# Optimization experiments

Hardware: AMD Instinct MI355X
Metric: run time of the kernel (lower is better)

## Reference

```python
import jax, jax.numpy as jnp
import numpy as np

N, E, D, L, G = 50000, 1600000, 128, 3, 64


def setup_inputs() -> dict:
    key = jax.random.key(0)
    ks = jax.random.split(key, 10)
    s = 1.0 / np.sqrt(D).astype(np.float32)
    X = jax.random.normal(ks[0], (N, D), jnp.float32)
    edge_index = jax.random.randint(ks[1], (2, E), 0, N, dtype=jnp.int32)
    edge_types = jax.random.randint(ks[2], (E,), 0, 2, dtype=jnp.int32)
    batch_ids = jnp.sort(jax.random.randint(ks[3], (N,), 0, G, dtype=jnp.int32))
    Wd = jax.random.uniform(ks[4], (L, D, D), jnp.float32, -s, s)
    bd = jax.random.uniform(ks[5], (L, D), jnp.float32, -s, s)
    Wc = jax.random.uniform(ks[6], (L, D, D), jnp.float32, -s, s)
    bc = jax.random.uniform(ks[7], (L, D), jnp.float32, -s, s)
    Ws = jax.random.uniform(ks[8], (L, D, D), jnp.float32, -s, s)
    bs = jax.random.uniform(ks[9], (L, D), jnp.float32, -s, s)
    return dict(X=X, Wd=Wd, bd=bd, Wc=Wc, bc=bc, Ws=Ws, bs=bs,
                edge_index=edge_index, edge_types=edge_types, batch_ids=batch_ids)


def reference(X, Wd, bd, Wc, bc, Ws, bs, edge_index, edge_types, batch_ids):
    src, dst = edge_index[0], edge_index[1]
    is_data = (edge_types == 0)[:, None]  # [E,1] edge-type selector
    for l in range(L):
        # Linear commutes with gather: compute node-level GEMMs once,
        # then per-edge gather + type select (same math as per-edge Linear).
        Xd = X @ Wd[l] + bd[l]            # [N,D] data-edge messages
        Xc = X @ Wc[l] + bc[l]            # [N,D] control-edge messages
        msg = jnp.where(is_data, Xd[src], Xc[src])      # [E,D]
        agg = jax.ops.segment_sum(msg, dst, num_segments=N)  # scatter-add
        X = jax.nn.relu(agg + X @ Ws[l] + bs[l])
    # global mean pool per graph
    sums = jax.ops.segment_sum(X, batch_ids, num_segments=G)
    cnts = jax.ops.segment_sum(jnp.ones((N,), X.dtype), batch_ids, num_segments=G)
    return sums / jnp.maximum(cnts, 1.0)[:, None]
```

## Files before the change

kernel.cpp:

```cpp
#include <hip/hip_runtime.h>
#include <hip/hip_fp16.h>

#define N_NODES 50000
#define N_EDGES 1600000
#define DIM     128
#define NLAYERS 3
#define NGRAPHS 64

#define NBUCK   196
#define CSR_BLKS 256
#define EPB     (N_EDGES / CSR_BLKS)
#define EITER   ((EPB + 255) / 256)

typedef _Float16 half8 __attribute__((ext_vector_type(8)));
typedef float    f32x4 __attribute__((ext_vector_type(4)));
typedef float    f32x2 __attribute__((ext_vector_type(2)));

#define LDK 136

__global__ __launch_bounds__(256) void setup_kernel(
        const float* __restrict__ X, __half* __restrict__ Xh,
        const float* __restrict__ Wd, const float* __restrict__ Wc,
        const float* __restrict__ Ws, __half* __restrict__ WT,
        float* __restrict__ sums, int* __restrict__ gcnt) {
    int i = blockIdx.x * 256 + threadIdx.x;
    if (i < N_NODES * DIM / 4) {
        float4 v = *(const float4*)(X + (size_t)i * 4);
        union { __half2 h2[2]; uint2 u; } pk;
        pk.h2[0] = __floats2half2_rn(v.x, v.y);
        pk.h2[1] = __floats2half2_rn(v.z, v.w);
        *(uint2*)(Xh + (size_t)i * 4) = pk.u;
    }
    if (i < 9 * DIM * DIM) {
        int k  = i & 127;
        int n  = (i >> 7) & 127;
        int lw = i >> 14;
        int l  = lw / 3, w = lw - 3 * l;
        const float* W = ((w == 0) ? Wd : (w == 1) ? Wc : Ws)
                         + (size_t)l * DIM * DIM;
        WT[i] = __float2half(W[k * DIM + n]);
    }
    if (i < NGRAPHS * DIM) sums[i] = 0.f;
    if (i < NGRAPHS) gcnt[i] = 0;
}

__global__ __launch_bounds__(256) void csr1_kernel(const int* __restrict__ dst,
                                                   int* __restrict__ cntmat) {
    __shared__ int hc[NBUCK];
    int tid = threadIdx.x;
    for (int i = tid; i < NBUCK; i += 256) hc[i] = 0;
    __syncthreads();
    int base = blockIdx.x * EPB;
#pragma unroll
    for (int i = 0; i < EITER; ++i) {
        int idx = i * 256 + tid;
        if (idx < EPB) atomicAdd(&hc[dst[base + idx] >> 8], 1);
    }
    __syncthreads();
    for (int i = tid; i < NBUCK; i += 256)
        cntmat[i * CSR_BLKS + blockIdx.x] = hc[i];
}

__global__ __launch_bounds__(256) void scanA_kernel(const int* __restrict__ cntmat,
                                                    int* __restrict__ exc,
                                                    int* __restrict__ btot) {
    __shared__ int sh[256];
    int tid = threadIdx.x, b = blockIdx.x;
    int v = cntmat[b * CSR_BLKS + tid];
    sh[tid] = v;
    __syncthreads();
    for (int o = 1; o < 256; o <<= 1) {
        int t = (tid >= o) ? sh[tid - o] : 0;
        __syncthreads();
        sh[tid] += t;
        __syncthreads();
    }
    exc[b * CSR_BLKS + tid] = sh[tid] - v;
    if (tid == 255) btot[b] = sh[255];
}

__global__ __launch_bounds__(256) void csr2_kernel(const int* __restrict__ src,
                                                   const int* __restrict__ dst,
                                                   const int* __restrict__ et,
                                                   const int* __restrict__ exc,
                                                   const int* __restrict__ btot,
                                                   int* __restrict__ bstart,
                                                   int* __restrict__ esv) {
    __shared__ int sh[256];
    __shared__ int bst[NBUCK];
    __shared__ int cur[NBUCK];
    int tid = threadIdx.x;
    int v = (tid < NBUCK) ? btot[tid] : 0;
    sh[tid] = v;
    __syncthreads();
    for (int o = 1; o < 256; o <<= 1) {
        int t = (tid >= o) ? sh[tid - o] : 0;
        __syncthreads();
        sh[tid] += t;
        __syncthreads();
    }
    if (tid < NBUCK) bst[tid] = sh[tid] - v;
    if (blockIdx.x == 0) {
        if (tid < NBUCK) bstart[tid] = sh[tid] - v;
        if (tid == NBUCK - 1) bstart[NBUCK] = sh[tid];
    }
    __syncthreads();
    if (tid < NBUCK) cur[tid] = exc[tid * CSR_BLKS + blockIdx.x] + bst[tid];
    __syncthreads();
    int base = blockIdx.x * EPB;
#pragma unroll
    for (int i = 0; i < EITER; ++i) {
        int idx = i * 256 + tid;
        if (idx < EPB) {
            int e = base + idx;
            int d = dst[e];
            int pos = atomicAdd(&cur[d >> 8], 1);
            esv[pos] = (src[e] + et[e] * N_NODES) | ((d & 255) << 17);
        }
    }
}

__global__ __launch_bounds__(256) void csr3_kernel(const int* __restrict__ esv,
                                                   const int* __restrict__ bstart,
                                                   int* __restrict__ col,
                                                   int* __restrict__ row_start,
                                                   int* __restrict__ deg) {
    __shared__ int cnt[256];
    __shared__ int sh[256];
    __shared__ int cur[256];
    int tid = threadIdx.x, b = blockIdx.x;
    int bs = bstart[b], be = bstart[b + 1];
    cnt[tid] = 0;
    __syncthreads();
    for (int e = bs + tid; e < be; e += 256)
        atomicAdd(&cnt[(esv[e] >> 17) & 255], 1);
    __syncthreads();
    int v = cnt[tid];
    sh[tid] = v;
    __syncthreads();
    for (int o = 1; o < 256; o <<= 1) {
        int t = (tid >= o) ? sh[tid - o] : 0;
        __syncthreads();
        sh[tid] += t;
        __syncthreads();
    }
    int off  = sh[tid] - v;
    int node = (b << 8) + tid;
    if (node < N_NODES) {
        row_start[node] = bs + off;
        deg[node]       = v;
    }
    cur[tid] = bs + off;
    __syncthreads();
    for (int e = bs + tid; e < be; e += 256) {
        int pk  = esv[e];
        int nd  = (pk >> 17) & 255;
        int pos = atomicAdd(&cur[nd], 1);
        col[pos] = pk & 0x1FFFF;
    }
}

__global__ __launch_bounds__(256) void gemm3m_kernel(
        const __half* __restrict__ Xh,
        const __half* __restrict__ WTl,
        const float* __restrict__ bd, const float* __restrict__ bc,
        const float* __restrict__ bs,
        unsigned char* __restrict__ Od, unsigned char* __restrict__ Oc,
        __half* __restrict__ Sh) {
    __shared__ _Float16 As[64 * LDK];
    __shared__ _Float16 Bs[128 * LDK];

    const int tid = threadIdx.x;
    const int m0  = blockIdx.x * 64;
    const int w   = blockIdx.y;

#pragma unroll
    for (int i = 0; i < 4; ++i) {
        int c    = i * 256 + tid;
        int row  = c >> 4;
        int colh = (c & 15) * 8;
        uint4 v  = make_uint4(0u, 0u, 0u, 0u);
        int gr   = m0 + row;
        if (gr < N_NODES) v = *(const uint4*)(Xh + (size_t)gr * DIM + colh);
        *(uint4*)(As + row * LDK + colh) = v;
    }
    {
        const __half* Wt = WTl + (size_t)w * DIM * DIM;
#pragma unroll
        for (int i = 0; i < 8; ++i) {
            int c    = i * 256 + tid;
            int row  = c >> 4;
            int colh = (c & 15) * 8;
            uint4 v = *(const uint4*)(Wt + (size_t)row * DIM + colh);
            *(uint4*)(Bs + row * LDK + colh) = v;
        }
    }
    __syncthreads();

    const int wv = tid >> 6;
    const int l  = tid & 63;
    const int lm = l & 15;
    const int q  = l >> 4;

    const int fb0 = wv * 32 + q * 4;
    const int fb1 = fb0 + 16;

    const float* bias = (w == 0) ? bd : (w == 1) ? bc : bs;
    f32x4 acc[4][2];
    {
        f32x4 bi0 = *(const f32x4*)(bias + fb0);
        f32x4 bi1 = *(const f32x4*)(bias + fb1);
#pragma unroll
        for (int mt = 0; mt < 4; ++mt) {
            acc[mt][0] = bi0;
            acc[mt][1] = bi1;
        }
    }

#pragma unroll
    for (int ks = 0; ks < 4; ++ks) {
        int coff = ks * 32 + q * 8;
        half8 am[4];
#pragma unroll
        for (int mt = 0; mt < 4; ++mt)
            am[mt] = *(const half8*)(As + (mt * 16 + lm) * LDK + coff);
        half8 bb0 = *(const half8*)(Bs + (wv * 32 + lm) * LDK + coff);
        half8 bb1 = *(const half8*)(Bs + (wv * 32 + 16 + lm) * LDK + coff);
#pragma unroll
        for (int mt = 0; mt < 4; ++mt) {
            acc[mt][0] = __builtin_amdgcn_mfma_f32_16x16x32_f16(bb0, am[mt], acc[mt][0], 0, 0, 0);
            acc[mt][1] = __builtin_amdgcn_mfma_f32_16x16x32_f16(bb1, am[mt], acc[mt][1], 0, 0, 0);
        }
    }

    if (w < 2) {
        unsigned char* O = (w == 0) ? Od : Oc;
#pragma unroll
        for (int mt = 0; mt < 4; ++mt) {
            int row = m0 + mt * 16 + lm;
            if (row < N_NODES) {
                int q0 = __builtin_amdgcn_cvt_pk_fp8_f32(acc[mt][0][0], acc[mt][0][1], 0, false);
                q0 = __builtin_amdgcn_cvt_pk_fp8_f32(acc[mt][0][2], acc[mt][0][3], q0, true);
                int q1 = __builtin_amdgcn_cvt_pk_fp8_f32(acc[mt][1][0], acc[mt][1][1], 0, false);
                q1 = __builtin_amdgcn_cvt_pk_fp8_f32(acc[mt][1][2], acc[mt][1][3], q1, true);
                *(unsigned int*)(O + (size_t)row * DIM + fb0) = (unsigned)q0;
                *(unsigned int*)(O + (size_t)row * DIM + fb1) = (unsigned)q1;
            }
        }
    } else {
#pragma unroll
        for (int mt = 0; mt < 4; ++mt) {
            int row = m0 + mt * 16 + lm;
            if (row < N_NODES) {
                union { __half2 h2[2]; uint2 u; } p0, p1;
                p0.h2[0] = __floats2half2_rn(acc[mt][0][0], acc[mt][0][1]);
                p0.h2[1] = __floats2half2_rn(acc[mt][0][2], acc[mt][0][3]);
                p1.h2[0] = __floats2half2_rn(acc[mt][1][0], acc[mt][1][1]);
                p1.h2[1] = __floats2half2_rn(acc[mt][1][2], acc[mt][1][3]);
                *(uint2*)(Sh + (size_t)row * DIM + fb0) = p0.u;
                *(uint2*)(Sh + (size_t)row * DIM + fb1) = p1.u;
            }
        }
    }
}

__global__ __launch_bounds__(256) void agg_kernel(
        const int* __restrict__ row_start, const int* __restrict__ deg_arr,
        const int* __restrict__ col,
        const unsigned char* __restrict__ Xdc,
        const __half* __restrict__ Sh, __half* __restrict__ Xout) {
    int wave = (blockIdx.x * 256 + threadIdx.x) >> 6;
    int lane = threadIdx.x & 63;
    int grp  = lane >> 4;
    int l16  = lane & 15;
    int node = wave * 4 + grp;
    if (node >= N_NODES) return;

    int rs  = row_start[node];
    int deg = deg_arr[node];
    const size_t off = (size_t)l16 * 8;

    union { uint4 u; __half2 h2[4]; } sv;
    sv.u = *(const uint4*)(Sh + (size_t)node * DIM + off);

    float acc[8];
#pragma unroll
    for (int j = 0; j < 8; ++j) acc[j] = 0.f;

    if (deg > 0) {
        int dgm1 = deg - 1;
        int nb   = (deg + 7) >> 3;
        int p[8];
#pragma unroll
        for (int i = 0; i < 8; ++i)
            p[i] = col[rs + (i < deg ? i : dgm1)];
        for (int b = 0; b < nb; ++b) {
            int e0 = b * 8;
            uint2 v[8];
#pragma unroll
            for (int i = 0; i < 8; ++i)
                v[i] = *(const uint2*)(Xdc + (size_t)p[i] * DIM + off);
            int pn[8];
            if (b + 1 < nb) {
                int e1 = e0 + 8;
#pragma unroll
                for (int i = 0; i < 8; ++i) {
                    int idx = e1 + i;
                    pn[i] = col[rs + (idx < deg ? idx : dgm1)];
                }
            }
#pragma unroll
            for (int i = 0; i < 8; ++i) {
                if (e0 + i >= deg) { v[i].x = 0u; v[i].y = 0u; }
            }
#pragma unroll
            for (int i = 0; i < 8; ++i) {
                f32x2 f0 = __builtin_amdgcn_cvt_pk_f32_fp8(v[i].x, false);
                f32x2 f1 = __builtin_amdgcn_cvt_pk_f32_fp8(v[i].x, true);
                f32x2 f2 = __builtin_amdgcn_cvt_pk_f32_fp8(v[i].y, false);
                f32x2 f3 = __builtin_amdgcn_cvt_pk_f32_fp8(v[i].y, true);
                acc[0] += f0[0]; acc[1] += f0[1];
                acc[2] += f1[0]; acc[3] += f1[1];
                acc[4] += f2[0]; acc[5] += f2[1];
                acc[6] += f3[0]; acc[7] += f3[1];
            }
            if (b + 1 < nb) {
#pragma unroll
                for (int i = 0; i < 8; ++i) p[i] = pn[i];
            }
        }
    }

    float s[8];
#pragma unroll
    for (int j = 0; j < 4; ++j) {
        float2 f = __half22float2(sv.h2[j]);
        s[2 * j]     = f.x;
        s[2 * j + 1] = f.y;
    }

    union { __half2 h2[4]; uint4 u; } pk;
#pragma unroll
    for (int j = 0; j < 4; ++j) {
        float r0 = fmaxf(acc[2 * j]     + s[2 * j],     0.f);
        float r1 = fmaxf(acc[2 * j + 1] + s[2 * j + 1], 0.f);
        pk.h2[j] = __floats2half2_rn(r0, r1);
    }
    *(uint4*)(Xout + (size_t)node * DIM + off) = pk.u;
}

__global__ __launch_bounds__(256) void pool_kernel(const __half* __restrict__ X,
                                                   const int* __restrict__ bid,
                                                   float* __restrict__ sums,
                                                   int* __restrict__ gcnt) {
    __shared__ float acc[8][DIM];
    __shared__ int scnt[8];
    __shared__ int sgmin;
    int tid = threadIdx.x;
    for (int i = tid; i < 8 * DIM; i += 256) ((float*)acc)[i] = 0.f;
    if (tid < 8) scnt[tid] = 0;
    int n0 = blockIdx.x * 64;
    if (tid == 0) sgmin = bid[n0];
    __syncthreads();
    int gmin = sgmin;

    int s    = tid >> 5;
    int lane = tid & 31;
    int r0   = n0 + s * 8;

    int g[8];
    union { uint2 u; __half2 h2[2]; } v[8];
#pragma unroll
    for (int i = 0; i < 8; ++i) {
        int r = r0 + i;
        g[i] = (r < N_NODES) ? bid[r] : -1;
    }
#pragma unroll
    for (int i = 0; i < 8; ++i) {
        int r = r0 + i;
        if (r < N_NODES)
            v[i].u = *(const uint2*)(X + (size_t)r * DIM + lane * 4);
        else { v[i].u.x = 0u; v[i].u.y = 0u; }
    }

    float4 a = make_float4(0.f, 0.f, 0.f, 0.f);
    int cur = -1, run = 0;
#pragma unroll
    for (int i = 0; i < 8; ++i) {
        if (g[i] != cur) {
            if (cur >= 0) {
                int slot = cur - gmin;
                if (slot < 8) {
                    atomicAdd(&acc[slot][lane * 4 + 0], a.x);
                    atomicAdd(&acc[slot][lane * 4 + 1], a.y);
                    atomicAdd(&acc[slot][lane * 4 + 2], a.z);
                    atomicAdd(&acc[slot][lane * 4 + 3], a.w);
                    if (lane == 0) atomicAdd(&scnt[slot], run);
                } else {
                    atomicAdd(&sums[cur * DIM + lane * 4 + 0], a.x);
                    atomicAdd(&sums[cur * DIM + lane * 4 + 1], a.y);
                    atomicAdd(&sums[cur * DIM + lane * 4 + 2], a.z);
                    atomicAdd(&sums[cur * DIM + lane * 4 + 3], a.w);
                    if (lane == 0) atomicAdd(&gcnt[cur], run);
                }
            }
            cur = g[i];
            a = make_float4(0.f, 0.f, 0.f, 0.f);
            run = 0;
        }
        if (g[i] >= 0) {
            float2 f0 = __half22float2(v[i].h2[0]);
            float2 f1 = __half22float2(v[i].h2[1]);
            a.x += f0.x; a.y += f0.y; a.z += f1.x; a.w += f1.y;
            run++;
        }
    }
    if (cur >= 0) {
        int slot = cur - gmin;
        if (slot < 8) {
            atomicAdd(&acc[slot][lane * 4 + 0], a.x);
            atomicAdd(&acc[slot][lane * 4 + 1], a.y);
            atomicAdd(&acc[slot][lane * 4 + 2], a.z);
            atomicAdd(&acc[slot][lane * 4 + 3], a.w);
            if (lane == 0) atomicAdd(&scnt[slot], run);
        } else {
            atomicAdd(&sums[cur * DIM + lane * 4 + 0], a.x);
            atomicAdd(&sums[cur * DIM + lane * 4 + 1], a.y);
            atomicAdd(&sums[cur * DIM + lane * 4 + 2], a.z);
            atomicAdd(&sums[cur * DIM + lane * 4 + 3], a.w);
            if (lane == 0) atomicAdd(&gcnt[cur], run);
        }
    }
    __syncthreads();

    for (int slot = 0; slot < 8; ++slot) {
        if (scnt[slot] > 0) {
            int gg = gmin + slot;
            for (int i = tid; i < DIM; i += 256)
                atomicAdd(&sums[gg * DIM + i], acc[slot][i]);
            if (tid == 0) atomicAdd(&gcnt[gg], scnt[slot]);
        }
    }
}

__global__ __launch_bounds__(256) void div_kernel(const float* __restrict__ sums,
                                                  const int* __restrict__ gcnt,
                                                  float* __restrict__ out) {
    int i = blockIdx.x * 256 + threadIdx.x;
    if (i < NGRAPHS * DIM) {
        int g = i >> 7;
        out[i] = sums[i] / fmaxf((float)gcnt[g], 1.f);
    }
}

extern "C" void kernel_launch(void* const* d_in, const int* in_sizes, int n_in,
                              void* d_out, int out_size, void* d_ws, size_t ws_size,
                              hipStream_t stream) {
    const float* Xin = (const float*)d_in[0];
    const float* Wd  = (const float*)d_in[1];
    const float* bd  = (const float*)d_in[2];
    const float* Wc  = (const float*)d_in[3];
    const float* bc  = (const float*)d_in[4];
    const float* Ws  = (const float*)d_in[5];
    const float* bs  = (const float*)d_in[6];
    const int* edge_index = (const int*)d_in[7];
    const int* edge_types = (const int*)d_in[8];
    const int* batch_ids  = (const int*)d_in[9];

    const int* src = edge_index;
    const int* dst = edge_index + N_EDGES;

    const size_t NBH = (size_t)N_NODES * DIM * sizeof(__half);
    const size_t NB8 = (size_t)N_NODES * DIM;
    char* w = (char*)d_ws;
    auto take = [&](size_t bytes) {
        char* p = w;
        w += (bytes + 255) & ~(size_t)255;
        return p;
    };
    __half* X0h  = (__half*)take(NBH);
    __half* Xb0h = (__half*)take(NBH);
    __half* Xb1h = (__half*)take(NBH);
    unsigned char* Xdc = (unsigned char*)take(2 * NB8);
    __half* Shb  = (__half*)take(NBH);
    __half* WT   = (__half*)take((size_t)9 * DIM * DIM * sizeof(__half));
    int* col     = (int*)take((size_t)N_EDGES * 4);
    int* esv     = (int*)take((size_t)N_EDGES * 4);
    int* cntmat  = (int*)take((size_t)NBUCK * CSR_BLKS * 4);
    int* exc     = (int*)take((size_t)NBUCK * CSR_BLKS * 4);
    int* btot    = (int*)take((size_t)NBUCK * 4);
    int* bstart  = (int*)take((size_t)(NBUCK + 1) * 4);
    int* rowst   = (int*)take((size_t)N_NODES * 4);
    int* deg     = (int*)take((size_t)N_NODES * 4);
    float* sums  = (float*)take((size_t)NGRAPHS * DIM * 4);
    int* gcnt    = (int*)take(NGRAPHS * 4);

    setup_kernel<<<(N_NODES * DIM / 4 + 255) / 256, 256, 0, stream>>>(
        Xin, X0h, Wd, Wc, Ws, WT, sums, gcnt);

    csr1_kernel<<<CSR_BLKS, 256, 0, stream>>>(dst, cntmat);
    scanA_kernel<<<NBUCK, 256, 0, stream>>>(cntmat, exc, btot);
    csr2_kernel<<<CSR_BLKS, 256, 0, stream>>>(src, dst, edge_types, exc,
                                              btot, bstart, esv);
    csr3_kernel<<<NBUCK, 256, 0, stream>>>(esv, bstart, col, rowst, deg);

    const int GEMM_MBLK = (N_NODES + 63) / 64;
    const int AGG_BLKS  = (N_NODES + 15) / 16;
    const __half* Xcur = X0h;
    __half* bufs[3] = {Xb0h, Xb1h, Xb0h};
    for (int l = 0; l < NLAYERS; ++l) {
        gemm3m_kernel<<<dim3(GEMM_MBLK, 3), 256, 0, stream>>>(
            Xcur, WT + (size_t)l * 3 * DIM * DIM,
            bd + (size_t)l * DIM, bc + (size_t)l * DIM, bs + (size_t)l * DIM,
            Xdc, Xdc + NB8, Shb);
        __half* Xnext = bufs[l];
        agg_kernel<<<AGG_BLKS, 256, 0, stream>>>(rowst, deg, col, Xdc, Shb, Xnext);
        Xcur = Xnext;
    }

    const int POOL_BLKS = (N_NODES + 63) / 64;
    pool_kernel<<<POOL_BLKS, 256, 0, stream>>>(Xcur, batch_ids, sums, gcnt);
    div_kernel<<<(NGRAPHS * DIM + 255) / 256, 256, 0, stream>>>(sums, gcnt,
                                                                (float*)d_out);
}
```

Baseline: 312.8 us.

## Sort nodes by degree for load-balanced aggregation wavefronts

Builds a degree-bucketed node permutation with a histogram, a scan and a scatter, and has the aggregation kernel process nodes in that order. Nodes sharing a wave then have similar degree, which cuts divergence from uneven edge loops. The cost is two extra small kernels, an extra indirection per node, and scattered reads and writes of node rows in aggregation, which loses the locality of the natural node order. The atomic scatter that fills the permutation also makes node order within a bucket nondeterministic.

```diff
diff --git a/kernel.cpp b/kernel.cpp
--- a/kernel.cpp
+++ b/kernel.cpp
@@ -11,6 +11,7 @@
 #define CSR_BLKS 256
 #define EPB     (N_EDGES / CSR_BLKS)
 #define EITER   ((EPB + 255) / 256)
+#define NBINS   256
 
 typedef _Float16 half8 __attribute__((ext_vector_type(8)));
 typedef float    f32x4 __attribute__((ext_vector_type(4)));
@@ -22,7 +23,8 @@
         const float* __restrict__ X, __half* __restrict__ Xh,
         const float* __restrict__ Wd, const float* __restrict__ Wc,
         const float* __restrict__ Ws, __half* __restrict__ WT,
-        float* __restrict__ sums, int* __restrict__ gcnt) {
+        float* __restrict__ sums, int* __restrict__ gcnt,
+        int* __restrict__ dbins) {
     int i = blockIdx.x * 256 + threadIdx.x;
     if (i < N_NODES * DIM / 4) {
         float4 v = *(const float4*)(X + (size_t)i * 4);
@@ -42,6 +44,7 @@
     }
     if (i < NGRAPHS * DIM) sums[i] = 0.f;
     if (i < NGRAPHS) gcnt[i] = 0;
+    if (i < NBINS) dbins[i] = 0;
 }
 
 __global__ __launch_bounds__(256) void csr1_kernel(const int* __restrict__ dst,
@@ -124,7 +127,8 @@
                                                    const int* __restrict__ bstart,
                                                    int* __restrict__ col,
                                                    int* __restrict__ row_start,
-                                                   int* __restrict__ deg) {
+                                                   int* __restrict__ deg,
+                                                   int* __restrict__ dbins) {
     __shared__ int cnt[256];
     __shared__ int sh[256];
     __shared__ int cur[256];
@@ -149,6 +153,7 @@
     if (node < N_NODES) {
         row_start[node] = bs + off;
         deg[node]       = v;
+        atomicAdd(&dbins[v & (NBINS - 1)], 1);
     }
     cur[tid] = bs + off;
     __syncthreads();
@@ -157,6 +162,32 @@
         int nd  = (pk >> 17) & 255;
         int pos = atomicAdd(&cur[nd], 1);
         col[pos] = pk & 0x1FFFF;
+    }
+}
+
+__global__ __launch_bounds__(256) void permA_kernel(const int* __restrict__ dbins,
+                                                    int* __restrict__ dcur) {
+    __shared__ int sh[256];
+    int tid = threadIdx.x;
+    int v = dbins[tid];
+    sh[tid] = v;
+    __syncthreads();
+    for (int o = 1; o < 256; o <<= 1) {
+        int t = (tid >= o) ? sh[tid - o] : 0;
+        __syncthreads();
+        sh[tid] += t;
+        __syncthreads();
+    }
+    dcur[tid] = sh[tid] - v;
+}
+
+__global__ __launch_bounds__(256) void permB_kernel(const int* __restrict__ deg,
+                                                    int* __restrict__ dcur,
+                                                    int* __restrict__ perm) {
+    int node = blockIdx.x * 256 + threadIdx.x;
+    if (node < N_NODES) {
+        int pos = atomicAdd(&dcur[deg[node] & (NBINS - 1)], 1);
+        perm[pos] = node;
     }
 }
 
@@ -266,15 +297,16 @@
 
 __global__ __launch_bounds__(256) void agg_kernel(
         const int* __restrict__ row_start, const int* __restrict__ deg_arr,
-        const int* __restrict__ col,
+        const int* __restrict__ perm, const int* __restrict__ col,
         const unsigned char* __restrict__ Xdc,
         const __half* __restrict__ Sh, __half* __restrict__ Xout) {
     int wave = (blockIdx.x * 256 + threadIdx.x) >> 6;
     int lane = threadIdx.x & 63;
     int grp  = lane >> 4;
     int l16  = lane & 15;
-    int node = wave * 4 + grp;
-    if (node >= N_NODES) return;
+    int gidx = wave * 4 + grp;
+    if (gidx >= N_NODES) return;
+    int node = perm[gidx];
 
     int rs  = row_start[node];
     int deg = deg_arr[node];
@@ -492,17 +524,22 @@
     int* bstart  = (int*)take((size_t)(NBUCK + 1) * 4);
     int* rowst   = (int*)take((size_t)N_NODES * 4);
     int* deg     = (int*)take((size_t)N_NODES * 4);
+    int* perm    = (int*)take((size_t)N_NODES * 4);
+    int* dbins   = (int*)take((size_t)NBINS * 4);
+    int* dcur    = (int*)take((size_t)NBINS * 4);
     float* sums  = (float*)take((size_t)NGRAPHS * DIM * 4);
     int* gcnt    = (int*)take(NGRAPHS * 4);
 
     setup_kernel<<<(N_NODES * DIM / 4 + 255) / 256, 256, 0, stream>>>(
-        Xin, X0h, Wd, Wc, Ws, WT, sums, gcnt);
+        Xin, X0h, Wd, Wc, Ws, WT, sums, gcnt, dbins);
 
     csr1_kernel<<<CSR_BLKS, 256, 0, stream>>>(dst, cntmat);
     scanA_kernel<<<NBUCK, 256, 0, stream>>>(cntmat, exc, btot);
     csr2_kernel<<<CSR_BLKS, 256, 0, stream>>>(src, dst, edge_types, exc,
                                               btot, bstart, esv);
-    csr3_kernel<<<NBUCK, 256, 0, stream>>>(esv, bstart, col, rowst, deg);
+    csr3_kernel<<<NBUCK, 256, 0, stream>>>(esv, bstart, col, rowst, deg, dbins);
+    permA_kernel<<<1, 256, 0, stream>>>(dbins, dcur);
+    permB_kernel<<<(N_NODES + 255) / 256, 256, 0, stream>>>(deg, dcur, perm);
 
     const int GEMM_MBLK = (N_NODES + 63) / 64;
     const int AGG_BLKS  = (N_NODES + 15) / 16;
@@ -514,7 +551,8 @@
             bd + (size_t)l * DIM, bc + (size_t)l * DIM, bs + (size_t)l * DIM,
             Xdc, Xdc + NB8, Shb);
         __half* Xnext = bufs[l];
-        agg_kernel<<<AGG_BLKS, 256, 0, stream>>>(rowst, deg, col, Xdc, Shb, Xnext);
+        agg_kernel<<<AGG_BLKS, 256, 0, stream>>>(rowst, deg, perm, col, Xdc,
+                                                 Shb, Xnext);
         Xcur = Xnext;
     }
 
```

After: 509.7 us. +63.0%, slower.
